# Kernel tuning notes

Hardware: AMD Instinct MI355X
Metric: run time of the kernel (lower is better)

Reference implementation:

```python
import jax, jax.numpy as jnp
import numpy as np

IN_FEATURES = 4096
OUT_FEATURES = 768
N_BITS = 8
SCALE = float(2 ** N_BITS - 1)  # 255
REG_WEIGHT = 0.001


def setup_inputs() -> dict:
    key = jax.random.key(0)
    k1, k2, k3 = jax.random.split(key, 3)
    latent = jax.random.normal(k1, (1024, IN_FEATURES), dtype=jnp.float32)
    true_sum = jax.random.uniform(k2, (1024, OUT_FEATURES * N_BITS), dtype=jnp.float32)
    # nn.init.uniform_(weight, -0.1, 0.1)
    weight = jax.random.uniform(k3, (IN_FEATURES, OUT_FEATURES * N_BITS),
                                dtype=jnp.float32, minval=-0.1, maxval=0.1)
    return {"latent": latent, "true_sum": true_sum, "weight": weight}


def _powers():
    # [1, 2, 4, ..., 2^(n-1)] with the top (sign) bit negated -> two's complement
    p = 2.0 ** jnp.arange(N_BITS, dtype=jnp.float32)
    return p.at[-1].multiply(-1.0)


def reference(latent, true_sum, weight):
    prob_weights = jax.nn.sigmoid(weight)                      # [in, out*n_bits]
    # min(|p-0|, |p-1|) = min(p, 1-p) for p in (0,1)
    reg_loss = REG_WEIGHT * jnp.minimum(prob_weights, 1.0 - prob_weights).mean()

    powers = _powers()                                         # [n_bits]
    int_weights = jnp.einsum('iob,b->io',
                             prob_weights.reshape(IN_FEATURES, -1, N_BITS),
                             powers)                           # [in, out]
    int_sum = jnp.einsum('nob,b->no',
                         true_sum.reshape(true_sum.shape[0], -1, N_BITS),
                         powers)                               # [B, out]

    # (latent[:, :, None] * int_weights[None]).sum(-2) == latent @ int_weights
    pred = jnp.einsum('bi,io->bo', latent, int_weights)        # [B, out]

    recon_loss = jnp.mean((pred / SCALE - int_sum / SCALE) ** 2)
    return (recon_loss + reg_loss, recon_loss, reg_loss)
```

## Files before the change

kernel.cpp:

```cpp
#include <hip/hip_runtime.h>
#include <hip/hip_bf16.h>
#include <stdint.h>

#define IN_F   4096
#define OUT_F  768
#define OUTB   (OUT_F * 8)
#define BATCH  1024
#define SPLITK 4
#define KSPAN  (IN_F / SPLITK)
#define BK     64
#define NIT    (KSPAN / BK)
#define PLANE  (BATCH * OUT_F)
#define PLANE4 (PLANE / 4)
#define EPIBLK 768

typedef short short8  __attribute__((ext_vector_type(8)));
typedef float f32x4   __attribute__((ext_vector_type(4)));
typedef unsigned int u32;

#define WS_WP    12582912
#define WS_LABF  18874368
#define WS_REGP  27262976
#define WS_SQP   27269120

__device__ __forceinline__ ushort f2bf(float f) {
    uint32_t u = __builtin_bit_cast(uint32_t, f);
    u += 0x7FFFu + ((u >> 16) & 1u);
    return (ushort)(u >> 16);
}

__device__ __forceinline__ float waveReduceSum(float v) {
    #pragma unroll
    for (int off = 32; off > 0; off >>= 1) v += __shfl_down(v, off, 64);
    return v;
}

__device__ __forceinline__ void glds16(const void* g, void* l) {
    __builtin_amdgcn_global_load_lds(
        (const __attribute__((address_space(1))) u32*)g,
        (__attribute__((address_space(3))) u32*)l, 16, 0, 0);
}

__global__ __launch_bounds__(256) void k_weights(const float* __restrict__ w,
                                                 const float* __restrict__ latent,
                                                 ushort* __restrict__ wp,
                                                 ushort* __restrict__ labf,
                                                 float* __restrict__ regpart) {
    if (blockIdx.x >= 1536) {
        int t = (blockIdx.x - 1536) * 256 + threadIdx.x;
        const float4* src = (const float4*)latent;
        uint4* dst = (uint4*)labf;
        #pragma unroll
        for (int j = 0; j < 4; j++) {
            int o = j * 131072 + t;
            float4 a0 = src[2 * o];
            float4 a1 = src[2 * o + 1];
            union { ushort u[8]; uint4 v; } pk;
            pk.u[0] = f2bf(a0.x); pk.u[1] = f2bf(a0.y); pk.u[2] = f2bf(a0.z); pk.u[3] = f2bf(a0.w);
            pk.u[4] = f2bf(a1.x); pk.u[5] = f2bf(a1.y); pk.u[6] = f2bf(a1.z); pk.u[7] = f2bf(a1.w);
            dst[o] = pk.v;
        }
        return;
    }

    int t  = blockIdx.x * 256 + threadIdx.x;
    int o  = t % OUT_F;
    int i8 = t / OUT_F;
    const float* src = w + (size_t)(i8 * 8) * OUTB + (size_t)o * 8;

    const float P[8] = {1.f, 2.f, 4.f, 8.f, 16.f, 32.f, 64.f, -128.f};
    float regsum = 0.f;
    union { ushort u[8]; uint4 v; } pk;

    #pragma unroll
    for (int r = 0; r < 8; r++) {
        float4 a = *(const float4*)(src + (size_t)r * OUTB);
        float4 b = *(const float4*)(src + (size_t)r * OUTB + 4);
        float x[8] = {a.x, a.y, a.z, a.w, b.x, b.y, b.z, b.w};
        float iw = 0.f;
        #pragma unroll
        for (int j = 0; j < 8; j++) {
            float p = __builtin_amdgcn_rcpf(1.f + __expf(-x[j]));
            iw += p * P[j];
            regsum += fminf(p, 1.f - p);
        }
        pk.u[r] = f2bf(iw);
    }
    *(uint4*)(wp + ((size_t)i8 * OUT_F + o) * 8) = pk.v;

    float ws = waveReduceSum(regsum);
    __shared__ float red[4];
    int lane = threadIdx.x & 63, wv = threadIdx.x >> 6;
    if (lane == 0) red[wv] = ws;
    __syncthreads();
    if (threadIdx.x == 0) regpart[blockIdx.x] = red[0] + red[1] + red[2] + red[3];
}

__global__ __launch_bounds__(256) void k_gemm(const ushort* __restrict__ labf,
                                              const ushort* __restrict__ wp,
                                              float* __restrict__ predp) {
    __shared__ __align__(16) ushort lA[2][64 * 72];
    __shared__ __align__(16) ushort lB[2][8 * 1032];

    const int tid  = threadIdx.x;
    const int n0   = blockIdx.x * 64;
    const int m0   = blockIdx.y * 64;
    const int bz   = blockIdx.z;
    const int kbase = bz * KSPAN;
    const int kg0   = kbase >> 3;
    const int lane = tid & 63, w = tid >> 6;
    const int wm = w >> 1, wn = w & 1;
    const int quad = lane >> 4, l16 = lane & 15;

    f32x4 acc[2][2] = {{{0.f,0.f,0.f,0.f},{0.f,0.f,0.f,0.f}},
                       {{0.f,0.f,0.f,0.f},{0.f,0.f,0.f,0.f}}};

    const int ar = tid >> 2, ac = tid & 3;
    const ushort* aptr = labf + (size_t)(m0 + ar) * IN_F + kbase + ac * 16;
    const ushort* bbase = wp + ((size_t)kg0 * OUT_F + n0 + lane) * 8;

    int buf = 0;
    glds16(bbase + (size_t)(2 * w) * OUT_F * 8,     &lB[0][(2 * w) * 1032]);
    glds16(bbase + (size_t)(2 * w + 1) * OUT_F * 8, &lB[0][(2 * w + 1) * 1032]);
    {
        uint4 a0 = *(const uint4*)aptr;
        uint4 a1 = *(const uint4*)(aptr + 8);
        *(uint4*)&lA[0][ar * 72 + ac * 16]     = a0;
        *(uint4*)&lA[0][ar * 72 + ac * 16 + 8] = a1;
    }
    __syncthreads();

    for (int it = 0; it < NIT; ++it) {
        const int nxt = buf ^ 1;
        uint4 a0, a1;
        if (it + 1 < NIT) {
            const ushort* bp = bbase + (size_t)(it + 1) * 8 * OUT_F * 8;
            glds16(bp + (size_t)(2 * w) * OUT_F * 8,     &lB[nxt][(2 * w) * 1032]);
            glds16(bp + (size_t)(2 * w + 1) * OUT_F * 8, &lB[nxt][(2 * w + 1) * 1032]);
            a0 = *(const uint4*)(aptr + (it + 1) * BK);
            a1 = *(const uint4*)(aptr + (it + 1) * BK + 8);
        }
        #pragma unroll
        for (int s = 0; s < 2; ++s) {
            short8 af0 = *(short8*)&lA[buf][(wm * 32 + l16) * 72 + s * 32 + quad * 8];
            short8 af1 = *(short8*)&lA[buf][(wm * 32 + 16 + l16) * 72 + s * 32 + quad * 8];
            short8 bf0 = *(short8*)&lB[buf][(s * 4 + quad) * 1032 + (wn * 32 + l16) * 8];
            short8 bf1 = *(short8*)&lB[buf][(s * 4 + quad) * 1032 + (wn * 32 + 16 + l16) * 8];
            acc[0][0] = __builtin_amdgcn_mfma_f32_16x16x32_bf16(af0, bf0, acc[0][0], 0, 0, 0);
            acc[0][1] = __builtin_amdgcn_mfma_f32_16x16x32_bf16(af0, bf1, acc[0][1], 0, 0, 0);
            acc[1][0] = __builtin_amdgcn_mfma_f32_16x16x32_bf16(af1, bf0, acc[1][0], 0, 0, 0);
            acc[1][1] = __builtin_amdgcn_mfma_f32_16x16x32_bf16(af1, bf1, acc[1][1], 0, 0, 0);
        }
        if (it + 1 < NIT) {
            *(uint4*)&lA[nxt][ar * 72 + ac * 16]     = a0;
            *(uint4*)&lA[nxt][ar * 72 + ac * 16 + 8] = a1;
        }
        __syncthreads();
        buf = nxt;
    }

    float* plane = predp + (size_t)bz * PLANE;
    #pragma unroll
    for (int fm = 0; fm < 2; fm++)
    #pragma unroll
    for (int fn = 0; fn < 2; fn++)
    #pragma unroll
    for (int r = 0; r < 4; r++) {
        int m = m0 + wm * 32 + fm * 16 + quad * 4 + r;
        int n = n0 + wn * 32 + fn * 16 + l16;
        plane[(size_t)m * OUT_F + n] = acc[fm][fn][r];
    }
}

__global__ __launch_bounds__(256) void k_epi(const float* __restrict__ predp,
                                             const float* __restrict__ tsum,
                                             float* __restrict__ sqpart) {
    int g = blockIdx.x * 256 + threadIdx.x;
    int m = g / (OUT_F / 4);
    int c = g % (OUT_F / 4);
    const float4* pp = (const float4*)predp;
    float4 p0 = pp[g];
    float4 p1 = pp[g + PLANE4];
    float4 p2 = pp[g + 2 * PLANE4];
    float4 p3 = pp[g + 3 * PLANE4];
    float pv[4] = {p0.x + p1.x + p2.x + p3.x, p0.y + p1.y + p2.y + p3.y,
                   p0.z + p1.z + p2.z + p3.z, p0.w + p1.w + p2.w + p3.w};
    const float* ts = tsum + (size_t)m * OUTB + (size_t)c * 32;
    float lsum = 0.f;
    #pragma unroll
    for (int j = 0; j < 4; j++) {
        float4 t0 = *(const float4*)(ts + j * 8);
        float4 t1 = *(const float4*)(ts + j * 8 + 4);
        float isum = t0.x + 2.f * t0.y + 4.f * t0.z + 8.f * t0.w
                   + 16.f * t1.x + 32.f * t1.y + 64.f * t1.z - 128.f * t1.w;
        float d = pv[j] - isum;
        lsum += d * d;
    }
    float wsum = waveReduceSum(lsum);
    __shared__ float red[4];
    if ((threadIdx.x & 63) == 0) red[threadIdx.x >> 6] = wsum;
    __syncthreads();
    if (threadIdx.x == 0)
        sqpart[blockIdx.x] = red[0] + red[1] + red[2] + red[3];
}

__global__ __launch_bounds__(256) void k_fin(const float* __restrict__ regpart,
                                             const float* __restrict__ sqpart,
                                             float* __restrict__ out) {
    int tid = threadIdx.x;
    float r = 0.f, s = 0.f;
    #pragma unroll
    for (int j = 0; j < 6; j++) r += regpart[tid + j * 256];
    #pragma unroll
    for (int j = 0; j < 3; j++) s += sqpart[tid + j * 256];
    r = waveReduceSum(r);
    s = waveReduceSum(s);
    __shared__ float redR[4], redS[4];
    int lane = tid & 63, wv = tid >> 6;
    if (lane == 0) { redR[wv] = r; redS[wv] = s; }
    __syncthreads();
    if (tid == 0) {
        float R = redR[0] + redR[1] + redR[2] + redR[3];
        float S = redS[0] + redS[1] + redS[2] + redS[3];
        float recon = S / ((float)(BATCH * OUT_F) * 255.f * 255.f);
        float reg   = 0.001f * R / (float)((size_t)IN_F * OUTB);
        out[0] = recon + reg;
        out[1] = recon;
        out[2] = reg;
    }
}

extern "C" void kernel_launch(void* const* d_in, const int* in_sizes, int n_in,
                              void* d_out, int out_size, void* d_ws, size_t ws_size,
                              hipStream_t stream) {
    const float* latent = (const float*)d_in[0];
    const float* tsum   = (const float*)d_in[1];
    const float* weight = (const float*)d_in[2];
    float* out      = (float*)d_out;
    float* predp    = (float*)d_ws;
    ushort* wp      = (ushort*)((char*)d_ws + WS_WP);
    ushort* labf    = (ushort*)((char*)d_ws + WS_LABF);
    float* regpart  = (float*)((char*)d_ws + WS_REGP);
    float* sqpart   = (float*)((char*)d_ws + WS_SQP);

    k_weights<<<2048, 256, 0, stream>>>(weight, latent, wp, labf, regpart);
    k_gemm<<<dim3(OUT_F / 64, BATCH / 64, SPLITK), 256, 0, stream>>>(labf, wp, predp);
    k_epi<<<EPIBLK, 256, 0, stream>>>(predp, tsum, sqpart);
    k_fin<<<1, 256, 0, stream>>>(regpart, sqpart, out);
}
```

Measured before the change: 200.9 us.

## Pre-pack latent into k-group-major layout and load MFMA fragments directly from global

After: 201.1 us. About the same (+0.1%).

```diff
diff --git a/kernel.cpp b/kernel.cpp
--- a/kernel.cpp
+++ b/kernel.cpp
@@ -8,18 +8,17 @@
 #define BATCH  1024
 #define SPLITK 4
 #define KSPAN  (IN_F / SPLITK)
-#define BK     64
-#define NIT    (KSPAN / BK)
+#define KGSPAN (KSPAN / 8)
+#define NIT    (KSPAN / 64)
 #define PLANE  (BATCH * OUT_F)
 #define PLANE4 (PLANE / 4)
 #define EPIBLK 768
 
 typedef short short8  __attribute__((ext_vector_type(8)));
 typedef float f32x4   __attribute__((ext_vector_type(4)));
-typedef unsigned int u32;
 
 #define WS_WP    12582912
-#define WS_LABF  18874368
+#define WS_LAT   18874368
 #define WS_REGP  27262976
 #define WS_SQP   27269120
 
@@ -35,30 +34,24 @@
     return v;
 }
 
-__device__ __forceinline__ void glds16(const void* g, void* l) {
-    __builtin_amdgcn_global_load_lds(
-        (const __attribute__((address_space(1))) u32*)g,
-        (__attribute__((address_space(3))) u32*)l, 16, 0, 0);
-}
-
 __global__ __launch_bounds__(256) void k_weights(const float* __restrict__ w,
                                                  const float* __restrict__ latent,
                                                  ushort* __restrict__ wp,
-                                                 ushort* __restrict__ labf,
+                                                 ushort* __restrict__ laT,
                                                  float* __restrict__ regpart) {
     if (blockIdx.x >= 1536) {
         int t = (blockIdx.x - 1536) * 256 + threadIdx.x;
-        const float4* src = (const float4*)latent;
-        uint4* dst = (uint4*)labf;
+        int m = t & 1023;
+        int kg0 = (t >> 10) << 2;
+        const float4* src = (const float4*)(latent + (size_t)m * IN_F + kg0 * 8);
         #pragma unroll
         for (int j = 0; j < 4; j++) {
-            int o = j * 131072 + t;
-            float4 a0 = src[2 * o];
-            float4 a1 = src[2 * o + 1];
+            float4 x0 = src[2 * j];
+            float4 x1 = src[2 * j + 1];
             union { ushort u[8]; uint4 v; } pk;
-            pk.u[0] = f2bf(a0.x); pk.u[1] = f2bf(a0.y); pk.u[2] = f2bf(a0.z); pk.u[3] = f2bf(a0.w);
-            pk.u[4] = f2bf(a1.x); pk.u[5] = f2bf(a1.y); pk.u[6] = f2bf(a1.z); pk.u[7] = f2bf(a1.w);
-            dst[o] = pk.v;
+            pk.u[0] = f2bf(x0.x); pk.u[1] = f2bf(x0.y); pk.u[2] = f2bf(x0.z); pk.u[3] = f2bf(x0.w);
+            pk.u[4] = f2bf(x1.x); pk.u[5] = f2bf(x1.y); pk.u[6] = f2bf(x1.z); pk.u[7] = f2bf(x1.w);
+            *(uint4*)(laT + (((size_t)(kg0 + j) << 10) + m) * 8) = pk.v;
         }
         return;
     }
@@ -96,18 +89,27 @@
     if (threadIdx.x == 0) regpart[blockIdx.x] = red[0] + red[1] + red[2] + red[3];
 }
 
-__global__ __launch_bounds__(256) void k_gemm(const ushort* __restrict__ labf,
-                                              const ushort* __restrict__ wp,
-                                              float* __restrict__ predp) {
-    __shared__ __align__(16) ushort lA[2][64 * 72];
-    __shared__ __align__(16) ushort lB[2][8 * 1032];
-
+#define LOAD_SET(A_, B_, it) do {                                              \
+    _Pragma("unroll") for (int s_ = 0; s_ < 2; s_++) {                         \
+        _Pragma("unroll") for (int f_ = 0; f_ < 2; f_++) {                     \
+            A_[s_][f_] = *(const short8*)(aB + (size_t)((it) * 8 + s_ * 4) * 8192 + f_ * 128); \
+            B_[s_][f_] = *(const short8*)(bB + (size_t)((it) * 8 + s_ * 4) * 6144 + f_ * 128); \
+        } } } while (0)
+
+#define MFMA_SET(A_, B_) do {                                                  \
+    _Pragma("unroll") for (int s_ = 0; s_ < 2; s_++)                           \
+    _Pragma("unroll") for (int fm_ = 0; fm_ < 2; fm_++)                        \
+    _Pragma("unroll") for (int fn_ = 0; fn_ < 2; fn_++)                        \
+        acc[fm_][fn_] = __builtin_amdgcn_mfma_f32_16x16x32_bf16(               \
+            A_[s_][fm_], B_[s_][fn_], acc[fm_][fn_], 0, 0, 0); } while (0)
+
+__global__ __launch_bounds__(256, 3) void k_gemm(const ushort* __restrict__ laT,
+                                                 const ushort* __restrict__ wp,
+                                                 float* __restrict__ predp) {
     const int tid  = threadIdx.x;
     const int n0   = blockIdx.x * 64;
     const int m0   = blockIdx.y * 64;
-    const int bz   = blockIdx.z;
-    const int kbase = bz * KSPAN;
-    const int kg0   = kbase >> 3;
+    const int kgb  = blockIdx.z * KGSPAN;
     const int lane = tid & 63, w = tid >> 6;
     const int wm = w >> 1, wn = w & 1;
     const int quad = lane >> 4, l16 = lane & 15;
@@ -115,51 +117,20 @@
     f32x4 acc[2][2] = {{{0.f,0.f,0.f,0.f},{0.f,0.f,0.f,0.f}},
                        {{0.f,0.f,0.f,0.f},{0.f,0.f,0.f,0.f}}};
 
-    const int ar = tid >> 2, ac = tid & 3;
-    const ushort* aptr = labf + (size_t)(m0 + ar) * IN_F + kbase + ac * 16;
-    const ushort* bbase = wp + ((size_t)kg0 * OUT_F + n0 + lane) * 8;
-
-    int buf = 0;
-    glds16(bbase + (size_t)(2 * w) * OUT_F * 8,     &lB[0][(2 * w) * 1032]);
-    glds16(bbase + (size_t)(2 * w + 1) * OUT_F * 8, &lB[0][(2 * w + 1) * 1032]);
-    {
-        uint4 a0 = *(const uint4*)aptr;
-        uint4 a1 = *(const uint4*)(aptr + 8);
-        *(uint4*)&lA[0][ar * 72 + ac * 16]     = a0;
-        *(uint4*)&lA[0][ar * 72 + ac * 16 + 8] = a1;
-    }
-    __syncthreads();
-
-    for (int it = 0; it < NIT; ++it) {
-        const int nxt = buf ^ 1;
-        uint4 a0, a1;
-        if (it + 1 < NIT) {
-            const ushort* bp = bbase + (size_t)(it + 1) * 8 * OUT_F * 8;
-            glds16(bp + (size_t)(2 * w) * OUT_F * 8,     &lB[nxt][(2 * w) * 1032]);
-            glds16(bp + (size_t)(2 * w + 1) * OUT_F * 8, &lB[nxt][(2 * w + 1) * 1032]);
-            a0 = *(const uint4*)(aptr + (it + 1) * BK);
-            a1 = *(const uint4*)(aptr + (it + 1) * BK + 8);
-        }
-        #pragma unroll
-        for (int s = 0; s < 2; ++s) {
-            short8 af0 = *(short8*)&lA[buf][(wm * 32 + l16) * 72 + s * 32 + quad * 8];
-            short8 af1 = *(short8*)&lA[buf][(wm * 32 + 16 + l16) * 72 + s * 32 + quad * 8];
-            short8 bf0 = *(short8*)&lB[buf][(s * 4 + quad) * 1032 + (wn * 32 + l16) * 8];
-            short8 bf1 = *(short8*)&lB[buf][(s * 4 + quad) * 1032 + (wn * 32 + 16 + l16) * 8];
-            acc[0][0] = __builtin_amdgcn_mfma_f32_16x16x32_bf16(af0, bf0, acc[0][0], 0, 0, 0);
-            acc[0][1] = __builtin_amdgcn_mfma_f32_16x16x32_bf16(af0, bf1, acc[0][1], 0, 0, 0);
-            acc[1][0] = __builtin_amdgcn_mfma_f32_16x16x32_bf16(af1, bf0, acc[1][0], 0, 0, 0);
-            acc[1][1] = __builtin_amdgcn_mfma_f32_16x16x32_bf16(af1, bf1, acc[1][1], 0, 0, 0);
-        }
-        if (it + 1 < NIT) {
-            *(uint4*)&lA[nxt][ar * 72 + ac * 16]     = a0;
-            *(uint4*)&lA[nxt][ar * 72 + ac * 16 + 8] = a1;
-        }
-        __syncthreads();
-        buf = nxt;
-    }
-
-    float* plane = predp + (size_t)bz * PLANE;
+    const ushort* aB = laT + (((size_t)(kgb + quad) << 10) + m0 + wm * 32 + l16) * 8;
+    const ushort* bB = wp  + ((size_t)(kgb + quad) * OUT_F + n0 + wn * 32 + l16) * 8;
+
+    short8 a0[2][2], b0[2][2], a1[2][2], b1[2][2];
+    LOAD_SET(a0, b0, 0);
+    #pragma unroll
+    for (int it = 0; it < NIT; it += 2) {
+        LOAD_SET(a1, b1, it + 1);
+        MFMA_SET(a0, b0);
+        if (it + 2 < NIT) LOAD_SET(a0, b0, it + 2);
+        MFMA_SET(a1, b1);
+    }
+
+    float* plane = predp + (size_t)blockIdx.z * PLANE;
     #pragma unroll
     for (int fm = 0; fm < 2; fm++)
     #pragma unroll
@@ -239,12 +210,12 @@
     float* out      = (float*)d_out;
     float* predp    = (float*)d_ws;
     ushort* wp      = (ushort*)((char*)d_ws + WS_WP);
-    ushort* labf    = (ushort*)((char*)d_ws + WS_LABF);
+    ushort* laT     = (ushort*)((char*)d_ws + WS_LAT);
     float* regpart  = (float*)((char*)d_ws + WS_REGP);
     float* sqpart   = (float*)((char*)d_ws + WS_SQP);
 
-    k_weights<<<2048, 256, 0, stream>>>(weight, latent, wp, labf, regpart);
-    k_gemm<<<dim3(OUT_F / 64, BATCH / 64, SPLITK), 256, 0, stream>>>(labf, wp, predp);
+    k_weights<<<2048, 256, 0, stream>>>(weight, latent, wp, laT, regpart);
+    k_gemm<<<dim3(OUT_F / 64, BATCH / 64, SPLITK), 256, 0, stream>>>(laT, wp, predp);
     k_epi<<<EPIBLK, 256, 0, stream>>>(predp, tsum, sqpart);
     k_fin<<<1, 256, 0, stream>>>(regpart, sqpart, out);
 }
```
